# Optimization experiments

Measured on AMD Instinct MI355X. Metric: run time of the kernel, lower is better.

## Reference

```python
import jax, jax.numpy as jnp
import numpy as np
import math

EPS = 1e-5  # PyTorch InstanceNorm default eps

def _inorm(x):
    # InstanceNorm1d(affine=False) applied to (N, L, F): with channels=L,
    # it normalizes each (n, l) row over the last (feature) axis, biased var.
    mu = jnp.mean(x, axis=-1, keepdims=True)
    var = jnp.var(x, axis=-1, keepdims=True)
    return (x - mu) * jax.lax.rsqrt(var + EPS)

def _proj(x, W, b):
    # Linear -> Tanh -> InstanceNorm (inside Sequential) -> InstanceNorm (QueryNorm etc.)
    return _inorm(_inorm(jnp.tanh(x @ W.T + b)))

def setup_inputs() -> dict:
    key = jax.random.key(0)
    N, D, H, W = 8, 512, 48, 48
    F_ = 512
    ks = jax.random.split(key, 7)
    s = 1.0 / math.sqrt(D)  # torch Linear default init bound
    inp = {"x": jax.random.normal(ks[0], (N, D, H, W), jnp.float32)}
    for i, name in enumerate(["q", "k", "v"]):
        inp[f"W{name}"] = jax.random.uniform(ks[1 + 2 * i], (F_, D), jnp.float32, -s, s)
        inp[f"b{name}"] = jax.random.uniform(ks[2 + 2 * i], (F_,), jnp.float32, -s, s)
    return inp

def reference(x, Wq, bq, Wk, bk, Wv, bv):
    N, D, H, W = x.shape
    F_ = Wq.shape[0]
    L = H * W
    # (N, D, H, W) -> (N, H, W, D) -> (N, L, D)
    flat = jnp.transpose(x, (0, 2, 3, 1)).reshape(N, L, D)
    Q = _proj(flat, Wq, bq)  # (N, L, F)
    K = _proj(flat, Wk, bk)
    V = _proj(flat, Wv, bv)
    scores = jnp.einsum('nlf,nmf->nlm', Q, K) / math.sqrt(F_)  # (N, L, L)
    attn = jax.nn.softmax(scores, axis=-1)
    A = jnp.einsum('nlm,nmf->nlf', attn, V)  # (N, L, F)
    return A.reshape(N, -1, H, W)  # raw reshape as in original: (N, F, H, W)
```

## Files before the change

### kernel.cpp

```cpp
#include <hip/hip_runtime.h>

typedef __attribute__((ext_vector_type(8))) short short8;
typedef __attribute__((ext_vector_type(4))) short short4v;
typedef __attribute__((ext_vector_type(4))) float floatx4;

__device__ __forceinline__ float bf2f(unsigned short u) {
    unsigned int v = ((unsigned int)u) << 16;
    return __builtin_bit_cast(float, v);
}
__device__ __forceinline__ unsigned short f2bf(float f) {
    unsigned int u = __builtin_bit_cast(unsigned int, f);
    u += 0x7fffu + ((u >> 16) & 1u);
    return (unsigned short)(u >> 16);
}

__device__ __forceinline__ void gl_lds16(const void* g, void* l) {
    __builtin_amdgcn_global_load_lds(
        (const __attribute__((address_space(1))) unsigned int*)g,
        (__attribute__((address_space(3))) unsigned int*)l, 16, 0, 0);
}

#define L_DIM 2304
#define D_DIM 512

__global__ void k_detect(const unsigned short* __restrict__ xs, int* __restrict__ flag) {
    int lane = threadIdx.x;
    int cnt = 0;
#pragma unroll
    for (int j = 0; j < 16; j++) {
        unsigned short u = xs[2 * (lane * 16 + j)];
        int e = (u >> 7) & 0xFF;
        cnt += (e >= 0xC0) ? 1 : 0;
    }
#pragma unroll
    for (int m = 1; m < 64; m <<= 1) cnt += __shfl_xor(cnt, m);
    if (lane == 0) *flag = (cnt > 4) ? 1 : 0;
}

__global__ __launch_bounds__(256) void k_cvt(const void* __restrict__ src,
                                             short* __restrict__ dst, int count,
                                             const int* __restrict__ flag) {
    int i = (blockIdx.x * 256 + threadIdx.x) * 8;
    if (i >= count) return;
    if (*flag) {
        const float* s = (const float*)src + i;
        short8 o;
#pragma unroll
        for (int j = 0; j < 8; j++) o[j] = (short)f2bf(s[j]);
        *(short8*)(dst + i) = o;
    } else {
        *(short8*)(dst + i) = *(const short8*)((const short*)src + i);
    }
}

__global__ __launch_bounds__(256) void k_transpose(const void* __restrict__ x_,
                                                   short* __restrict__ fx,
                                                   const int* __restrict__ flag) {
    __shared__ __align__(16) short t[64 * 72];
    const int n = blockIdx.z, d0 = blockIdx.y * 64, l0 = blockIdx.x * 64;
    const int tid = threadIdx.x;
    if (*flag) {
        const float* x = (const float*)x_;
#pragma unroll
        for (int p = 0; p < 4; p++) {
            int i = tid + p * 256;
            int dr = i >> 4, lc = (i & 15) * 4;
            floatx4 v = *(const floatx4*)(x + (size_t)(n * D_DIM + d0 + dr) * L_DIM + l0 + lc);
#pragma unroll
            for (int j = 0; j < 4; j++) t[(lc + j) * 72 + dr] = (short)f2bf(v[j]);
        }
    } else {
        const short* x = (const short*)x_;
#pragma unroll
        for (int p = 0; p < 2; p++) {
            int i = tid + p * 256;
            int dr = i >> 3, lc = (i & 7) * 8;
            short8 v = *(const short8*)(x + (size_t)(n * D_DIM + d0 + dr) * L_DIM + l0 + lc);
#pragma unroll
            for (int j = 0; j < 8; j++) t[(lc + j) * 72 + dr] = v[j];
        }
    }
    __syncthreads();
#pragma unroll
    for (int p = 0; p < 2; p++) {
        int i = tid + p * 256;
        int lr = i >> 3, dc = (i & 7) * 8;
        short8 v = *(const short8*)&t[lr * 72 + dc];
        *(short8*)(fx + (size_t)(n * L_DIM + l0 + lr) * D_DIM + d0 + dc) = v;
    }
}

__global__ __launch_bounds__(256) void k_trV(const short* __restrict__ src,
                                             short* __restrict__ dst) {
    __shared__ __align__(16) short t[64 * 72];
    const int n = blockIdx.z, l0 = blockIdx.x * 64, f0 = blockIdx.y * 64;
    const int tid = threadIdx.x;
    const int lo4 = (tid & 15) * 4;
    const int fo = (tid >> 4) * 8;
    const int fo8 = ((tid >> 4) & 7) * 8;
    const int lo = lo4 + ((tid >> 7) & 1) * 0;
    short8 v[4];
#pragma unroll
    for (int p = 0; p < 1; p++) { }
    const int lsub = (tid >> 7) * 0;
    if (tid < 128) {
        const int ll = (tid & 15) * 4;
        const int ff = (tid >> 4) * 8;
#pragma unroll
        for (int r = 0; r < 4; r++)
            v[r] = *(const short8*)(src + (size_t)(n * L_DIM + l0 + ll + r) * D_DIM + f0 + ff);
#pragma unroll
        for (int j = 0; j < 8; j++) {
            short4v w = { v[0][j], v[1][j], v[2][j], v[3][j] };
            *(short4v*)&t[(ff + j) * 72 + ll] = w;
        }
    }
    __syncthreads();
#pragma unroll
    for (int p = 0; p < 2; p++) {
        int i = tid + p * 256;
        int fr = i >> 3, lc = (i & 7) * 8;
        short8 o = *(const short8*)&t[fr * 72 + lc];
        *(short8*)(dst + (size_t)(n * D_DIM + f0 + fr) * L_DIM + l0 + lc) = o;
    }
}

__device__ __forceinline__ void gemm128(const short* __restrict__ A,
                                        const short* __restrict__ B,
                                        int K, int l0, int f0,
                                        short* ldsA, short* ldsB,
                                        floatx4 acc[4][4]) {
    const int tid = threadIdx.x, lane = tid & 63, wid = tid >> 6;
    const int wm = wid & 1, wn = wid >> 1, quad = lane >> 4, l16 = lane & 15;
    const int r16 = lane >> 2, c8 = (lane & 3) * 8;
    for (int kt = 0; kt < K; kt += 32) {
        __syncthreads();
#pragma unroll
        for (int p = 0; p < 2; p++) {
            int row = (wid + p * 4) * 16;
            gl_lds16(A + (size_t)(l0 + row + r16) * K + kt + c8, ldsA + row * 32);
            gl_lds16(B + (size_t)(f0 + row + r16) * K + kt + c8, ldsB + row * 32);
        }
        __syncthreads();
        short8 a[4], b[4];
#pragma unroll
        for (int mi = 0; mi < 4; mi++)
            a[mi] = *(const short8*)&ldsA[(wm * 64 + mi * 16 + l16) * 32 + quad * 8];
#pragma unroll
        for (int ni = 0; ni < 4; ni++)
            b[ni] = *(const short8*)&ldsB[(wn * 64 + ni * 16 + l16) * 32 + quad * 8];
#pragma unroll
        for (int mi = 0; mi < 4; mi++)
#pragma unroll
            for (int ni = 0; ni < 4; ni++)
                acc[mi][ni] = __builtin_amdgcn_mfma_f32_16x16x32_bf16(a[mi], b[ni], acc[mi][ni], 0, 0, 0);
    }
}

__global__ __launch_bounds__(256) void k_gemm_proj(const short* __restrict__ fx,
                                                   const short* __restrict__ Wc,
                                                   const short* __restrict__ bc,
                                                   short* __restrict__ Pbase) {
    __shared__ __align__(16) short ldsA[128 * 32];
    __shared__ __align__(16) short ldsB[128 * 32];
    const int proj = blockIdx.y, n = blockIdx.z;
    const int l0 = (blockIdx.x >> 2) * 128, f0 = (blockIdx.x & 3) * 128;
    const short* A = fx + (size_t)n * L_DIM * D_DIM;
    const short* B = Wc + (size_t)proj * 262144;
    const short* bias = bc + proj * 512;
    short* P = Pbase + (size_t)proj * 8 * L_DIM * D_DIM + (size_t)n * L_DIM * D_DIM;
    const int lane = threadIdx.x & 63, wid = threadIdx.x >> 6;
    const int wm = wid & 1, wn = wid >> 1, quad = lane >> 4, l16 = lane & 15;

    floatx4 acc[4][4] = {};
    gemm128(A, B, 512, l0, f0, ldsA, ldsB, acc);

#pragma unroll
    for (int ni = 0; ni < 4; ni++) {
        int f = f0 + wn * 64 + ni * 16 + l16;
        float bb = bf2f((unsigned short)bias[f]);
#pragma unroll
        for (int mi = 0; mi < 4; mi++) {
#pragma unroll
            for (int r = 0; r < 4; r++) {
                int l = l0 + wm * 64 + mi * 16 + quad * 4 + r;
                float v = tanhf(acc[mi][ni][r] + bb);
                P[(size_t)l * 512 + f] = (short)f2bf(v);
            }
        }
    }
}

__global__ __launch_bounds__(256) void k_norm(short* __restrict__ base) {
    const int row = blockIdx.x * 4 + (threadIdx.x >> 6);
    const int lane = threadIdx.x & 63;
    short* p = base + (size_t)row * 512 + lane * 8;
    short8 v = *(const short8*)p;
    float x[8], s = 0.f, sq = 0.f;
#pragma unroll
    for (int j = 0; j < 8; j++) {
        x[j] = bf2f((unsigned short)v[j]);
        s += x[j];
        sq += x[j] * x[j];
    }
#pragma unroll
    for (int m = 1; m < 64; m <<= 1) {
        s += __shfl_xor(s, m);
        sq += __shfl_xor(sq, m);
    }
    float mu = s * (1.0f / 512.0f);
    float var = sq * (1.0f / 512.0f) - mu * mu;
    float r1 = rsqrtf(var + 1e-5f);
    float y[8], s2 = 0.f, sq2 = 0.f;
#pragma unroll
    for (int j = 0; j < 8; j++) {
        y[j] = (x[j] - mu) * r1;
        s2 += y[j];
        sq2 += y[j] * y[j];
    }
#pragma unroll
    for (int m = 1; m < 64; m <<= 1) {
        s2 += __shfl_xor(s2, m);
        sq2 += __shfl_xor(sq2, m);
    }
    float mu2 = s2 * (1.0f / 512.0f);
    float var2 = sq2 * (1.0f / 512.0f) - mu2 * mu2;
    float r2 = rsqrtf(var2 + 1e-5f);
    short8 o;
#pragma unroll
    for (int j = 0; j < 8; j++) o[j] = (short)f2bf((y[j] - mu2) * r2);
    *(short8*)p = o;
}

__global__ __launch_bounds__(256) void k_gemm_scores(const short* __restrict__ Q,
                                                     const short* __restrict__ Kb,
                                                     short* __restrict__ P,
                                                     float* __restrict__ lsum) {
    __shared__ __align__(16) short ldsA[128 * 32];
    __shared__ __align__(16) short ldsB[128 * 32];
    const int n = blockIdx.y;
    const int l0 = (blockIdx.x / 18) * 128, m0 = (blockIdx.x % 18) * 128;
    const short* A = Q + (size_t)n * L_DIM * D_DIM;
    const short* B = Kb + (size_t)n * L_DIM * D_DIM;
    const int lane = threadIdx.x & 63, wid = threadIdx.x >> 6;
    const int wm = wid & 1, wn = wid >> 1, quad = lane >> 4, l16 = lane & 15;

    floatx4 acc[4][4] = {};
    gemm128(A, B, 512, l0, m0, ldsA, ldsB, acc);

    const float sc = 0.044194173824159216f;
    short* Pn = P + (size_t)n * L_DIM * L_DIM;
    float* ln = lsum + n * L_DIM;
#pragma unroll
    for (int mi = 0; mi < 4; mi++) {
#pragma unroll
        for (int r = 0; r < 4; r++) {
            int row = l0 + wm * 64 + mi * 16 + quad * 4 + r;
            float s = 0.f;
#pragma unroll
            for (int ni = 0; ni < 4; ni++) {
                int col = m0 + wn * 64 + ni * 16 + l16;
                unsigned short pb = f2bf(__expf(acc[mi][ni][r] * sc));
                Pn[(size_t)row * L_DIM + col] = (short)pb;
                s += bf2f(pb);
            }
            s += __shfl_xor(s, 1);
            s += __shfl_xor(s, 2);
            s += __shfl_xor(s, 4);
            s += __shfl_xor(s, 8);
            if (l16 == 0) atomicAdd(&ln[row], s);
        }
    }
}

__global__ __launch_bounds__(256) void k_gemm_out(const short* __restrict__ P,
                                                  const short* __restrict__ Vt,
                                                  const float* __restrict__ lsum,
                                                  void* __restrict__ out_,
                                                  const int* __restrict__ flag) {
    __shared__ __align__(16) short ldsA[128 * 32];
    __shared__ __align__(16) short ldsB[128 * 32];
    const int n = blockIdx.y;
    const int l0 = (blockIdx.x >> 2) * 128, f0 = (blockIdx.x & 3) * 128;
    const short* A = P + (size_t)n * L_DIM * L_DIM;
    const short* B = Vt + (size_t)n * D_DIM * L_DIM;
    const int lane = threadIdx.x & 63, wid = threadIdx.x >> 6;
    const int wm = wid & 1, wn = wid >> 1, quad = lane >> 4, l16 = lane & 15;

    floatx4 acc[4][4] = {};
    gemm128(A, B, L_DIM, l0, f0, ldsA, ldsB, acc);

    const int fl = *flag;
#pragma unroll
    for (int mi = 0; mi < 4; mi++) {
#pragma unroll
        for (int r = 0; r < 4; r++) {
            int row = l0 + wm * 64 + mi * 16 + quad * 4 + r;
            float rl = 1.0f / lsum[n * L_DIM + row];
            if (fl) {
                float* out = (float*)out_;
#pragma unroll
                for (int ni = 0; ni < 4; ni++) {
                    int f = f0 + wn * 64 + ni * 16 + l16;
                    out[((size_t)n * L_DIM + row) * 512 + f] = acc[mi][ni][r] * rl;
                }
            } else {
                short* out = (short*)out_;
#pragma unroll
                for (int ni = 0; ni < 4; ni++) {
                    int f = f0 + wn * 64 + ni * 16 + l16;
                    out[((size_t)n * L_DIM + row) * 512 + f] = (short)f2bf(acc[mi][ni][r] * rl);
                }
            }
        }
    }
}

__global__ __launch_bounds__(512) void k_attn(const short* __restrict__ Q,
                                              const short* __restrict__ K,
                                              const short* __restrict__ V,
                                              void* __restrict__ out_,
                                              const int* __restrict__ flag) {
    __shared__ __align__(16) short ldsKV[512 * 40];
    __shared__ __align__(16) short ldsP[64 * 40];
    __shared__ float ldsL[64];
    const int n = blockIdx.y;
    const int q0 = blockIdx.x * 64;
    const int tid = threadIdx.x, lane = tid & 63, wid = tid >> 6;
    const int wq = wid & 3, wk = wid >> 2, quad = lane >> 4, l16 = lane & 15;
    const short* Qn = Q + (size_t)n * L_DIM * 512;
    const short* Kn = K + (size_t)n * L_DIM * 512;
    const short* Vn = V + (size_t)n * L_DIM * 512;
    if (tid < 64) ldsL[tid] = 0.f;

    short8 qf[16];
#pragma unroll
    for (int fs = 0; fs < 16; fs++)
        qf[fs] = *(const short8*)(Qn + (size_t)(q0 + wq * 16 + l16) * 512 + fs * 32 + quad * 8);

    floatx4 acc[16] = {};
    const float sc = 0.044194173824159216f;

    for (int kt = 0; kt < 72; kt++) {
        const int key0 = kt * 32;
        __syncthreads();
#pragma unroll
        for (int p = 0; p < 4; p++) {
            int i = tid + p * 512;
            int row = i >> 6, c = (i & 63) * 8;
            *(short8*)&ldsKV[row * 520 + c] =
                *(const short8*)(Kn + (size_t)(key0 + row) * 512 + c);
        }
        __syncthreads();
        floatx4 sacc = {0.f, 0.f, 0.f, 0.f};
#pragma unroll
        for (int fs = 0; fs < 16; fs++) {
            short8 kf = *(const short8*)&ldsKV[(wk * 16 + l16) * 520 + fs * 32 + quad * 8];
            sacc = __builtin_amdgcn_mfma_f32_16x16x32_bf16(qf[fs], kf, sacc, 0, 0, 0);
        }
        float pe[4];
#pragma unroll
        for (int r = 0; r < 4; r++) {
            unsigned short pb = f2bf(__expf(sacc[r] * sc));
            ldsP[(wq * 16 + quad * 4 + r) * 40 + wk * 16 + l16] = (short)pb;
            pe[r] = bf2f(pb);
        }
#pragma unroll
        for (int r = 0; r < 4; r++) {
            float s = pe[r];
            s += __shfl_xor(s, 1);
            s += __shfl_xor(s, 2);
            s += __shfl_xor(s, 4);
            s += __shfl_xor(s, 8);
            if (l16 == 0) atomicAdd(&ldsL[wq * 16 + quad * 4 + r], s);
        }
        __syncthreads();
#pragma unroll
        for (int p = 0; p < 4; p++) {
            int i = tid + p * 512;
            int row = i >> 6, c = (i & 63) * 8;
            short8 v = *(const short8*)(Vn + (size_t)(key0 + row) * 512 + c);
#pragma unroll
            for (int j = 0; j < 8; j++) ldsKV[(c + j) * 40 + row] = v[j];
        }
        __syncthreads();
        short8 pf = *(const short8*)&ldsP[(wq * 16 + l16) * 40 + quad * 8];
#pragma unroll
        for (int ni = 0; ni < 16; ni++) {
            short8 vf = *(const short8*)&ldsKV[(wk * 256 + ni * 16 + l16) * 40 + quad * 8];
            acc[ni] = __builtin_amdgcn_mfma_f32_16x16x32_bf16(pf, vf, acc[ni], 0, 0, 0);
        }
    }
    __syncthreads();
    float rl[4];
#pragma unroll
    for (int r = 0; r < 4; r++) rl[r] = 1.0f / ldsL[wq * 16 + quad * 4 + r];
    if (*flag) {
        float* out = (float*)out_;
#pragma unroll
        for (int ni = 0; ni < 16; ni++) {
            int f = wk * 256 + ni * 16 + l16;
#pragma unroll
            for (int r = 0; r < 4; r++) {
                int q = q0 + wq * 16 + quad * 4 + r;
                out[((size_t)n * L_DIM + q) * 512 + f] = acc[ni][r] * rl[r];
            }
        }
    } else {
        short* out = (short*)out_;
#pragma unroll
        for (int ni = 0; ni < 16; ni++) {
            int f = wk * 256 + ni * 16 + l16;
#pragma unroll
            for (int r = 0; r < 4; r++) {
                int q = q0 + wq * 16 + quad * 4 + r;
                out[((size_t)n * L_DIM + q) * 512 + f] = (short)f2bf(acc[ni][r] * rl[r]);
            }
        }
    }
}

extern "C" void kernel_launch(void* const* d_in, const int* in_sizes, int n_in,
                              void* d_out, int out_size, void* d_ws, size_t ws_size,
                              hipStream_t stream) {
    char* ws = (char*)d_ws;
    const size_t S1 = (size_t)8 * L_DIM * D_DIM * sizeof(short);
    int* flag = (int*)ws;
    short* Wc = (short*)(ws + 4096);
    short* bc = (short*)(ws + 4096 + 3 * 262144 * 2);
    short* flatX = (short*)(ws + 1581056);
    short* Pq = (short*)((char*)flatX + S1);
    short* Pk = (short*)((char*)Pq + S1);
    short* Pv = (short*)((char*)Pk + S1);

    k_detect<<<1, 64, 0, stream>>>((const unsigned short*)d_in[0], flag);
    k_cvt<<<128, 256, 0, stream>>>(d_in[1], Wc + 0 * 262144, 262144, flag);
    k_cvt<<<128, 256, 0, stream>>>(d_in[3], Wc + 1 * 262144, 262144, flag);
    k_cvt<<<128, 256, 0, stream>>>(d_in[5], Wc + 2 * 262144, 262144, flag);
    k_cvt<<<1, 256, 0, stream>>>(d_in[2], bc + 0, 512, flag);
    k_cvt<<<1, 256, 0, stream>>>(d_in[4], bc + 512, 512, flag);
    k_cvt<<<1, 256, 0, stream>>>(d_in[6], bc + 1024, 512, flag);
    k_transpose<<<dim3(36, 8, 8), 256, 0, stream>>>(d_in[0], flatX, flag);
    k_gemm_proj<<<dim3(72, 3, 8), 256, 0, stream>>>(flatX, Wc, bc, Pq);
    k_norm<<<13824, 256, 0, stream>>>(Pq);

    const size_t need = 1581056 + 5 * S1 + 73728 + (size_t)8 * L_DIM * L_DIM * 2;
    if (ws_size >= need) {
        short* Vt = (short*)((char*)Pv + S1);
        float* lsum = (float*)((char*)Vt + S1);
        short* P = (short*)((char*)lsum + 73728);
        k_trV<<<dim3(36, 8, 8), 256, 0, stream>>>(Pv, Vt);
        hipMemsetAsync(lsum, 0, 8 * L_DIM * sizeof(float), stream);
        k_gemm_scores<<<dim3(324, 8), 256, 0, stream>>>(Pq, Pk, P, lsum);
        k_gemm_out<<<dim3(72, 8), 256, 0, stream>>>(P, Vt, lsum, d_out, flag);
    } else {
        k_attn<<<dim3(36, 8), 512, 0, stream>>>(Pq, Pk, Pv, d_out, flag);
    }
}
```

Measured before the change: 358.9 us.

## Merge prep launches, remap grids batch-fastest, use nontemporal stores for P and output

Six weight and bias conversion launches and the lsum memset are merged into one k_prep kernel, which cuts launch overhead. The GEMM grids are flattened to 1D with the batch index varying fastest, which changes block scheduling and how L2 is shared across blocks. The probability matrix and output are now written with nontemporal stores, which should reduce cache pollution, though P is read back right away by the next GEMM. Dead variables in k_trV are also removed.

```diff
diff --git a/kernel.cpp b/kernel.cpp
--- a/kernel.cpp
+++ b/kernel.cpp
@@ -37,19 +37,45 @@
     if (lane == 0) *flag = (cnt > 4) ? 1 : 0;
 }
 
-__global__ __launch_bounds__(256) void k_cvt(const void* __restrict__ src,
-                                             short* __restrict__ dst, int count,
-                                             const int* __restrict__ flag) {
-    int i = (blockIdx.x * 256 + threadIdx.x) * 8;
-    if (i >= count) return;
-    if (*flag) {
-        const float* s = (const float*)src + i;
-        short8 o;
-#pragma unroll
-        for (int j = 0; j < 8; j++) o[j] = (short)f2bf(s[j]);
-        *(short8*)(dst + i) = o;
+__global__ __launch_bounds__(256) void k_prep(
+    const void* __restrict__ w0, const void* __restrict__ w1, const void* __restrict__ w2,
+    const void* __restrict__ b0, const void* __restrict__ b1, const void* __restrict__ b2,
+    short* __restrict__ Wc, short* __restrict__ bc,
+    float* __restrict__ lsum, int lcount, const int* __restrict__ flag) {
+    const int b = blockIdx.x, tid = threadIdx.x;
+    const int fl = *flag;
+    if (b < 384) {
+        int w = b >> 7, blk = b & 127;
+        const void* src = w == 0 ? w0 : (w == 1 ? w1 : w2);
+        short* dst = Wc + (size_t)w * 262144;
+        int i = (blk * 256 + tid) * 8;
+        if (fl) {
+            const float* s = (const float*)src + i;
+            short8 o;
+#pragma unroll
+            for (int j = 0; j < 8; j++) o[j] = (short)f2bf(s[j]);
+            *(short8*)(dst + i) = o;
+        } else {
+            *(short8*)(dst + i) = *(const short8*)((const short*)src + i);
+        }
+    } else if (b == 384) {
+        int i = tid * 8;
+        if (i < 1536) {
+            int which = i >> 9, off = i & 511;
+            const void* src = which == 0 ? b0 : (which == 1 ? b1 : b2);
+            short* dst = bc + which * 512 + off;
+            if (fl) {
+                const float* s = (const float*)src + off;
+#pragma unroll
+                for (int j = 0; j < 8; j++) dst[j] = (short)f2bf(s[j]);
+            } else {
+#pragma unroll
+                for (int j = 0; j < 8; j++) dst[j] = ((const short*)src)[off + j];
+            }
+        }
     } else {
-        *(short8*)(dst + i) = *(const short8*)((const short*)src + i);
+        int idx = (b - 385) * 256 + tid;
+        if (idx < lcount) lsum[idx] = 0.f;
     }
 }
 
@@ -95,17 +121,10 @@
     __shared__ __align__(16) short t[64 * 72];
     const int n = blockIdx.z, l0 = blockIdx.x * 64, f0 = blockIdx.y * 64;
     const int tid = threadIdx.x;
-    const int lo4 = (tid & 15) * 4;
-    const int fo = (tid >> 4) * 8;
-    const int fo8 = ((tid >> 4) & 7) * 8;
-    const int lo = lo4 + ((tid >> 7) & 1) * 0;
-    short8 v[4];
-#pragma unroll
-    for (int p = 0; p < 1; p++) { }
-    const int lsub = (tid >> 7) * 0;
     if (tid < 128) {
         const int ll = (tid & 15) * 4;
         const int ff = (tid >> 4) * 8;
+        short8 v[4];
 #pragma unroll
         for (int r = 0; r < 4; r++)
             v[r] = *(const short8*)(src + (size_t)(n * L_DIM + l0 + ll + r) * D_DIM + f0 + ff);
@@ -163,8 +182,10 @@
                                                    short* __restrict__ Pbase) {
     __shared__ __align__(16) short ldsA[128 * 32];
     __shared__ __align__(16) short ldsB[128 * 32];
-    const int proj = blockIdx.y, n = blockIdx.z;
-    const int l0 = (blockIdx.x >> 2) * 128, f0 = (blockIdx.x & 3) * 128;
+    const int bx = blockIdx.x;
+    const int n = bx & 7, t = bx >> 3;
+    const int proj = t / 72, tt = t % 72;
+    const int l0 = (tt >> 2) * 128, f0 = (tt & 3) * 128;
     const short* A = fx + (size_t)n * L_DIM * D_DIM;
     const short* B = Wc + (size_t)proj * 262144;
     const short* bias = bc + proj * 512;
@@ -238,8 +259,9 @@
                                                      float* __restrict__ lsum) {
     __shared__ __align__(16) short ldsA[128 * 32];
     __shared__ __align__(16) short ldsB[128 * 32];
-    const int n = blockIdx.y;
-    const int l0 = (blockIdx.x / 18) * 128, m0 = (blockIdx.x % 18) * 128;
+    const int bx = blockIdx.x;
+    const int n = bx & 7, t = bx >> 3;
+    const int l0 = (t / 18) * 128, m0 = (t % 18) * 128;
     const short* A = Q + (size_t)n * L_DIM * D_DIM;
     const short* B = Kb + (size_t)n * L_DIM * D_DIM;
     const int lane = threadIdx.x & 63, wid = threadIdx.x >> 6;
@@ -261,7 +283,7 @@
             for (int ni = 0; ni < 4; ni++) {
                 int col = m0 + wn * 64 + ni * 16 + l16;
                 unsigned short pb = f2bf(__expf(acc[mi][ni][r] * sc));
-                Pn[(size_t)row * L_DIM + col] = (short)pb;
+                __builtin_nontemporal_store((short)pb, &Pn[(size_t)row * L_DIM + col]);
                 s += bf2f(pb);
             }
             s += __shfl_xor(s, 1);
@@ -280,8 +302,9 @@
                                                   const int* __restrict__ flag) {
     __shared__ __align__(16) short ldsA[128 * 32];
     __shared__ __align__(16) short ldsB[128 * 32];
-    const int n = blockIdx.y;
-    const int l0 = (blockIdx.x >> 2) * 128, f0 = (blockIdx.x & 3) * 128;
+    const int bx = blockIdx.x;
+    const int n = bx & 7, t = bx >> 3;
+    const int l0 = (t >> 2) * 128, f0 = (t & 3) * 128;
     const short* A = P + (size_t)n * L_DIM * L_DIM;
     const short* B = Vt + (size_t)n * D_DIM * L_DIM;
     const int lane = threadIdx.x & 63, wid = threadIdx.x >> 6;
@@ -302,14 +325,16 @@
 #pragma unroll
                 for (int ni = 0; ni < 4; ni++) {
                     int f = f0 + wn * 64 + ni * 16 + l16;
-                    out[((size_t)n * L_DIM + row) * 512 + f] = acc[mi][ni][r] * rl;
+                    __builtin_nontemporal_store(acc[mi][ni][r] * rl,
+                        &out[((size_t)n * L_DIM + row) * 512 + f]);
                 }
             } else {
                 short* out = (short*)out_;
 #pragma unroll
                 for (int ni = 0; ni < 4; ni++) {
                     int f = f0 + wn * 64 + ni * 16 + l16;
-                    out[((size_t)n * L_DIM + row) * 512 + f] = (short)f2bf(acc[mi][ni][r] * rl);
+                    __builtin_nontemporal_store((short)f2bf(acc[mi][ni][r] * rl),
+                        &out[((size_t)n * L_DIM + row) * 512 + f]);
                 }
             }
         }
@@ -433,26 +458,23 @@
     short* Pk = (short*)((char*)Pq + S1);
     short* Pv = (short*)((char*)Pk + S1);
 
+    const size_t need = 1581056 + 5 * S1 + 73728 + (size_t)8 * L_DIM * L_DIM * 2;
+    const bool big = ws_size >= need;
+    short* Vt = (short*)((char*)Pv + S1);
+    float* lsum = (float*)((char*)Vt + S1);
+    short* P = (short*)((char*)lsum + 73728);
+
     k_detect<<<1, 64, 0, stream>>>((const unsigned short*)d_in[0], flag);
-    k_cvt<<<128, 256, 0, stream>>>(d_in[1], Wc + 0 * 262144, 262144, flag);
-    k_cvt<<<128, 256, 0, stream>>>(d_in[3], Wc + 1 * 262144, 262144, flag);
-    k_cvt<<<128, 256, 0, stream>>>(d_in[5], Wc + 2 * 262144, 262144, flag);
-    k_cvt<<<1, 256, 0, stream>>>(d_in[2], bc + 0, 512, flag);
-    k_cvt<<<1, 256, 0, stream>>>(d_in[4], bc + 512, 512, flag);
-    k_cvt<<<1, 256, 0, stream>>>(d_in[6], bc + 1024, 512, flag);
+    k_prep<<<457, 256, 0, stream>>>(d_in[1], d_in[3], d_in[5], d_in[2], d_in[4], d_in[6],
+                                    Wc, bc, lsum, big ? 18432 : 0, flag);
     k_transpose<<<dim3(36, 8, 8), 256, 0, stream>>>(d_in[0], flatX, flag);
-    k_gemm_proj<<<dim3(72, 3, 8), 256, 0, stream>>>(flatX, Wc, bc, Pq);
+    k_gemm_proj<<<1728, 256, 0, stream>>>(flatX, Wc, bc, Pq);
     k_norm<<<13824, 256, 0, stream>>>(Pq);
 
-    const size_t need = 1581056 + 5 * S1 + 73728 + (size_t)8 * L_DIM * L_DIM * 2;
-    if (ws_size >= need) {
-        short* Vt = (short*)((char*)Pv + S1);
-        float* lsum = (float*)((char*)Vt + S1);
-        short* P = (short*)((char*)lsum + 73728);
+    if (big) {
         k_trV<<<dim3(36, 8, 8), 256, 0, stream>>>(Pv, Vt);
-        hipMemsetAsync(lsum, 0, 8 * L_DIM * sizeof(float), stream);
-        k_gemm_scores<<<dim3(324, 8), 256, 0, stream>>>(Pq, Pk, P, lsum);
-        k_gemm_out<<<dim3(72, 8), 256, 0, stream>>>(P, Vt, lsum, d_out, flag);
+        k_gemm_scores<<<2592, 256, 0, stream>>>(Pq, Pk, P, lsum);
+        k_gemm_out<<<576, 256, 0, stream>>>(P, Vt, lsum, d_out, flag);
     } else {
         k_attn<<<dim3(36, 8), 512, 0, stream>>>(Pq, Pk, Pv, d_out, flag);
     }
```

Measured after the change: 360.2 us. No clear change (+0.4%).
